# Kernel tuning notes

Hardware: AMD Instinct MI355X
Metric: run time of the kernel (lower is better)

## Reference

```python
import jax, jax.numpy as jnp
import numpy as np

NUM_CLS = 80
C = 256
IMG = 1024.0
N = 256
SR = 2  # sampling_ratio
MIN_SIZE = 16.0
SCALES = (0.25, 0.125, 0.0625, 0.03125)
HW = ((256, 256), (128, 128), (64, 64), (32, 32))


def _roialign(feat, rois, scale, out):
    # feat: [C, H, W]; rois: [n, 4] (y1, x1, y2, x2) in image coords.
    # torchvision-style ROIAlign (aligned=False), sampling_ratio=SR, avg pool.
    Cc, H, W = feat.shape
    n = rois.shape[0]
    y1 = rois[:, 0] * scale
    x1 = rois[:, 1] * scale
    rh = jnp.maximum(rois[:, 2] * scale - y1, 1.0)
    rw = jnp.maximum(rois[:, 3] * scale - x1, 1.0)
    # per-bin sample offsets: (bin + (s+0.5)/SR) * bin_size
    g = (jnp.arange(out, dtype=feat.dtype)[:, None]
         + (jnp.arange(SR, dtype=feat.dtype)[None, :] + 0.5) / SR).reshape(-1)  # [out*SR]
    ys = y1[:, None] + g[None, :] * (rh / out)[:, None]  # [n, out*SR]
    xs = x1[:, None] + g[None, :] * (rw / out)[:, None]
    S = out * SR
    yy = jnp.broadcast_to(ys[:, :, None], (n, S, S)).reshape(n, S * S)
    xx = jnp.broadcast_to(xs[:, None, :], (n, S, S)).reshape(n, S * S)
    valid = (yy > -1.0) & (yy < H) & (xx > -1.0) & (xx < W)
    yc = jnp.clip(yy, 0.0, H - 1.0)
    xc = jnp.clip(xx, 0.0, W - 1.0)
    y0 = jnp.floor(yc)
    x0 = jnp.floor(xc)
    ly = yc - y0
    lx = xc - x0
    y0i = y0.astype(jnp.int32)
    x0i = x0.astype(jnp.int32)
    y1i = jnp.minimum(y0i + 1, H - 1)
    x1i = jnp.minimum(x0i + 1, W - 1)
    f00 = feat[:, y0i, x0i]  # [C, n, S*S]
    f01 = feat[:, y0i, x1i]
    f10 = feat[:, y1i, x0i]
    f11 = feat[:, y1i, x1i]
    val = (f00 * (1 - ly) * (1 - lx) + f01 * (1 - ly) * lx
           + f10 * ly * (1 - lx) + f11 * ly * lx)
    val = jnp.where(valid[None], val, 0.0)
    val = val.reshape(Cc, n, out, SR, out, SR).mean(axis=(3, 5))
    return val.transpose(1, 0, 2, 3)  # [n, C, out, out]


def _pool(P, rois, out):
    # roi_layer: FPN level assignment via log2 of sqrt(area)/224, clamp to levels 0..3
    area = jnp.prod(rois[:, 2:4] - rois[:, 0:2] + 1.0, axis=-1)
    lvl = jnp.clip(jnp.floor(4.0 + jnp.log(jnp.sqrt(area) / 224.0) / np.log(2.0)), 2.0, 5.0) - 2.0
    lvl = lvl.astype(jnp.int32)
    pooled = jnp.zeros((rois.shape[0], C, out, out), dtype=rois.dtype)
    for l in range(4):
        pl = _roialign(P[l], rois, SCALES[l], out)
        pooled = pooled + jnp.where((lvl == l)[:, None, None, None], pl, 0.0)
    return pooled


def _loc2bbox(loc, anchor):
    chw = anchor[..., 2:4] - anchor[..., 0:2]
    cyx = anchor[..., 0:2] + chw * 0.5
    yx = loc[..., 0:2] * chw + cyx
    hw = jnp.exp(loc[..., 2:4]) * chw
    return jnp.concatenate([yx - hw * 0.5, yx + hw * 0.5], axis=-1)


def _head(x, W1, b1, W2, b2, Wc, bc, Wl, bl):
    x = x.reshape(x.shape[0], -1)
    h = jax.nn.relu(x @ W1 + b1)
    h = jax.nn.relu(h @ W2 + b2)
    return h @ Wc + bc, h @ Wl + bl


def _cascade(P, rois, params):
    stds = (jnp.array([0.1, 0.1, 0.2, 0.2], dtype=rois.dtype),
            jnp.array([0.05, 0.05, 0.1, 0.1], dtype=rois.dtype),
            jnp.array([1 / 30.0, 1 / 30.0, 1 / 15.0, 1 / 15.0], dtype=rois.dtype))
    roi = rois
    valid = jnp.ones((rois.shape[0],), dtype=bool)
    t = jnp.arange(rois.shape[0])
    pre_b = jnp.zeros((rois.shape[0], NUM_CLS, 4), dtype=rois.dtype)
    pre_s = jnp.zeros((rois.shape[0], NUM_CLS), dtype=rois.dtype)
    for s in range(3):
        x = _pool(P, roi, 7)
        logits, loc = _head(x, *params[s])
        loc = loc.reshape(-1, NUM_CLS + 1, 4)[:, 1:] * stds[s]
        boxes = _loc2bbox(loc, roi[:, None, :])  # [N, NUM_CLS, 4]
        score = jax.nn.softmax(logits, axis=-1)[:, 1:]
        pre_b = pre_b + boxes
        pre_s = pre_s + score
        best = jnp.argmax(score, axis=-1)
        roi = boxes[t, best]
        roi = jnp.clip(roi, 0.0, IMG)  # square image: clamp both coords to [0, IMG]
        if s < 2:  # original filters only after stages 1 and 2
            hw = roi[:, 2:4] - roi[:, 0:2]
            valid = valid & jnp.all(hw >= MIN_SIZE, axis=-1)
    m = valid.astype(pre_s.dtype)
    return pre_b / 3.0 * m[:, None, None], pre_s / 3.0 * m[:, None]


def setup_inputs():
    key = jax.random.key(0)
    ks = jax.random.split(key, 32)
    inp = {}
    for i, (h, w) in enumerate(HW):
        inp[f"P{i}"] = jax.random.normal(ks[i], (C, h, w), dtype=jnp.float32)
    yx1 = jax.random.uniform(ks[4], (N, 2), minval=0.0, maxval=IMG - 64.0)
    sz = jnp.exp(jax.random.uniform(ks[5], (N, 2), minval=np.log(16.0), maxval=np.log(600.0)))
    yx2 = jnp.clip(yx1 + sz, 0.0, IMG - 1.0)
    inp["rois"] = jnp.concatenate([yx1, yx2], axis=-1).astype(jnp.float32)
    dims = [(C * 49, 1024), (1024,), (1024, 1024), (1024,),
            (1024, NUM_CLS + 1), (NUM_CLS + 1,), (1024, (NUM_CLS + 1) * 4), ((NUM_CLS + 1) * 4,)]
    names = ["W1", "b1", "W2", "b2", "Wc", "bc", "Wl", "bl"]
    k = 6
    for s in range(3):
        for nm, d in zip(names, dims):
            if len(d) == 1:
                inp[f"s{s}_{nm}"] = jnp.zeros(d, dtype=jnp.float32)
            else:
                inp[f"s{s}_{nm}"] = 0.02 * jax.random.normal(ks[k], d, dtype=jnp.float32)
                k += 1
    return inp


def reference(P0, P1, P2, P3, rois,
              s0_W1, s0_b1, s0_W2, s0_b2, s0_Wc, s0_bc, s0_Wl, s0_bl,
              s1_W1, s1_b1, s1_W2, s1_b2, s1_Wc, s1_bc, s1_Wl, s1_bl,
              s2_W1, s2_b1, s2_W2, s2_b2, s2_Wc, s2_bc, s2_Wl, s2_bl):
    P = (P0, P1, P2, P3)
    params = [(s0_W1, s0_b1, s0_W2, s0_b2, s0_Wc, s0_bc, s0_Wl, s0_bl),
              (s1_W1, s1_b1, s1_W2, s1_b2, s1_Wc, s1_bc, s1_Wl, s1_bl),
              (s2_W1, s2_b1, s2_W2, s2_b2, s2_Wc, s2_bc, s2_Wl, s2_bl)]
    return _cascade(P, rois, params)
```

## Files before the change

kernel.cpp:

```cpp
#include <hip/hip_runtime.h>
#include <math.h>


#define NROI 256
#define NCLS 80
#define APITCH 40

typedef __attribute__((ext_vector_type(8))) short short8;
typedef __attribute__((ext_vector_type(4))) float f32x4;

__device__ __forceinline__ unsigned short f2bf(float f) {
  unsigned u = __builtin_bit_cast(unsigned, f);
  unsigned r = (u + 0x7FFFu + ((u >> 16) & 1u)) >> 16;
  return (unsigned short)r;
}
__device__ __forceinline__ float bf2f(unsigned short u) {
  return __builtin_bit_cast(float, (unsigned)u << 16);
}

__global__ __launch_bounds__(256) void prep_kernel(
    const float* __restrict__ P0, const float* __restrict__ P1,
    const float* __restrict__ P2, const float* __restrict__ P3,
    unsigned short* __restrict__ Pb0, unsigned short* __restrict__ Pb1,
    unsigned short* __restrict__ Pb2, unsigned short* __restrict__ Pb3,
    const float* __restrict__ W1a, const float* __restrict__ W1b,
    const float* __restrict__ W1c,
    const float* __restrict__ W2a, const float* __restrict__ W2b,
    const float* __restrict__ W2c,
    const float* __restrict__ Wca, const float* __restrict__ Wcb,
    const float* __restrict__ Wcc,
    const float* __restrict__ Wla, const float* __restrict__ Wlb,
    const float* __restrict__ Wlc,
    unsigned short* __restrict__ Wt1, unsigned short* __restrict__ Wt2,
    unsigned short* __restrict__ Wth) {
  __shared__ unsigned short lt[32][66];
  int bid = blockIdx.x;
  int t = threadIdx.x;
  int r0 = t >> 3;
  int c = t & 7;

  float4 v0, v1;
  unsigned short* D;
  size_t drow;
  int Kd;
  int k0;

  if (bid < 10880) {
    const float* S;
    int N, idx;
    if (bid < 8192)       { S = P0; D = Pb0; N = 65536; idx = bid; }
    else if (bid < 10240) { S = P1; D = Pb1; N = 16384; idx = bid - 8192; }
    else if (bid < 10752) { S = P2; D = Pb2; N = 4096;  idx = bid - 10240; }
    else                  { S = P3; D = Pb3; N = 1024;  idx = bid - 10752; }
    k0 = (idx & 3) * 64;
    int n0 = (idx >> 2) * 32;
    Kd = 256;
    drow = n0;
    const float* a = S + (size_t)(k0 + r0) * N + n0 + c * 4;
    v0 = *(const float4*)a;
    v1 = *(const float4*)(a + (size_t)32 * N);
  } else if (bid < 29696) {
    int idx = bid - 10880;
    int s = idx / 6272;
    idx -= s * 6272;
    const float* W = (s == 0) ? W1a : (s == 1) ? W1b : W1c;
    int kd0 = (idx % 196) * 64;
    int n0 = (idx / 196) * 32;
    int p = kd0 >> 8;
    int c0 = kd0 & 255;
    k0 = kd0;
    Kd = 12544;
    drow = n0;
    D = Wt1 + (size_t)s * 12544 * 1024;
    const float* a = W + (size_t)((c0 + r0) * 49 + p) * 1024 + n0 + c * 4;
    v0 = *(const float4*)a;
    v1 = *(const float4*)(a + (size_t)32 * 49 * 1024);
  } else if (bid < 31232) {
    int idx = bid - 29696;
    int s = idx >> 9;
    idx &= 511;
    const float* W = (s == 0) ? W2a : (s == 1) ? W2b : W2c;
    k0 = (idx & 15) * 64;
    int n0 = (idx >> 4) * 32;
    Kd = 1024;
    drow = n0;
    D = Wt2 + (size_t)s * 1024 * 1024;
    const float* a = W + (size_t)(k0 + r0) * 1024 + n0 + c * 4;
    v0 = *(const float4*)a;
    v1 = *(const float4*)(a + (size_t)32 * 1024);
  } else {
    int idx = bid - 31232;
    int s = idx >> 8;
    idx &= 255;
    const float* wc = (s == 0) ? Wca : (s == 1) ? Wcb : Wcc;
    const float* wl = (s == 0) ? Wla : (s == 1) ? Wlb : Wlc;
    k0 = (idx & 15) * 64;
    int n0 = (idx >> 4) * 32;
    Kd = 1024;
    drow = n0;
    D = Wth + (size_t)s * 512 * 1024;
    float a0[4], a1[4];
#pragma unroll
    for (int j = 0; j < 4; j++) {
      int nn = n0 + c * 4 + j;
      float x0 = 0.0f, x1 = 0.0f;
      if (nn < 81) {
        x0 = wc[(size_t)(k0 + r0) * 81 + nn];
        x1 = wc[(size_t)(k0 + r0 + 32) * 81 + nn];
      } else if (nn < 405) {
        x0 = wl[(size_t)(k0 + r0) * 324 + (nn - 81)];
        x1 = wl[(size_t)(k0 + r0 + 32) * 324 + (nn - 81)];
      }
      a0[j] = x0;
      a1[j] = x1;
    }
    v0.x = a0[0]; v0.y = a0[1]; v0.z = a0[2]; v0.w = a0[3];
    v1.x = a1[0]; v1.y = a1[1]; v1.z = a1[2]; v1.w = a1[3];
  }

  const float* pv0 = (const float*)&v0;
  const float* pv1 = (const float*)&v1;
#pragma unroll
  for (int j = 0; j < 4; j++) {
    lt[c * 4 + j][r0] = f2bf(pv0[j]);
    lt[c * 4 + j][r0 + 32] = f2bf(pv1[j]);
  }
  __syncthreads();

  int n = t >> 3;
  int k8 = (t & 7) * 8;
  const unsigned int* lrow = (const unsigned int*)&lt[n][k8];
  uint4 o;
  o.x = lrow[0];
  o.y = lrow[1];
  o.z = lrow[2];
  o.w = lrow[3];
  *(uint4*)(D + (drow + n) * (size_t)Kd + k0 + k8) = o;
}

__global__ __launch_bounds__(256) void pool_kernel2(
    const unsigned short* __restrict__ Pb0, const unsigned short* __restrict__ Pb1,
    const unsigned short* __restrict__ Pb2, const unsigned short* __restrict__ Pb3,
    const float* __restrict__ roi, unsigned short* __restrict__ pooled) {
  int t = threadIdx.x;
  int n = blockIdx.y;
  int p = blockIdx.x * 4 + (t >> 6);
  if (p >= 49) return;
  int lane = t & 63;
  int c4 = lane * 4;
  int py = p / 7, px = p % 7;

  float r0 = roi[n * 4 + 0];
  float r1 = roi[n * 4 + 1];
  float r2 = roi[n * 4 + 2];
  float r3 = roi[n * 4 + 3];

  float area = (r2 - r0 + 1.0f) * (r3 - r1 + 1.0f);
  float lf = floorf(4.0f + log2f(sqrtf(area) / 224.0f));
  lf = fminf(fmaxf(lf, 2.0f), 5.0f);
  int lvl = (int)lf - 2;

  float scale;
  int H;
  const unsigned short* fb;
  if (lvl == 0)      { scale = 0.25f;    H = 256; fb = Pb0; }
  else if (lvl == 1) { scale = 0.125f;   H = 128; fb = Pb1; }
  else if (lvl == 2) { scale = 0.0625f;  H = 64;  fb = Pb2; }
  else               { scale = 0.03125f; H = 32;  fb = Pb3; }
  int W = H;

  float y1 = r0 * scale;
  float x1 = r1 * scale;
  float rh = fmaxf(r2 * scale - y1, 1.0f);
  float rw = fmaxf(r3 * scale - x1, 1.0f);
  float bh = rh * (1.0f / 7.0f);
  float bw = rw * (1.0f / 7.0f);

  float a0 = 0.f, a1 = 0.f, a2 = 0.f, a3 = 0.f;
#pragma unroll
  for (int ry = 0; ry < 2; ry++) {
    float yy = y1 + ((float)py + ((float)ry + 0.5f) * 0.5f) * bh;
    bool vy = (yy > -1.0f) && (yy < (float)H);
    float ycl = fminf(fmaxf(yy, 0.0f), (float)(H - 1));
    float y0f = floorf(ycl);
    float ly = ycl - y0f;
    int y0i = (int)y0f;
    int y1i = min(y0i + 1, H - 1);
#pragma unroll
    for (int rx = 0; rx < 2; rx++) {
      float xx = x1 + ((float)px + ((float)rx + 0.5f) * 0.5f) * bw;
      bool vx = (xx > -1.0f) && (xx < (float)W);
      float xcl = fminf(fmaxf(xx, 0.0f), (float)(W - 1));
      float x0f = floorf(xcl);
      float lx = xcl - x0f;
      int x0i = (int)x0f;
      int x1i = min(x0i + 1, W - 1);
      float w00 = (1.f - ly) * (1.f - lx);
      float w01 = (1.f - ly) * lx;
      float w10 = ly * (1.f - lx);
      float w11 = ly * lx;
      if (!(vy && vx)) { w00 = w01 = w10 = w11 = 0.f; }
      ushort4 f00 = *(const ushort4*)(fb + ((size_t)(y0i * W + x0i) * 256 + c4));
      ushort4 f01 = *(const ushort4*)(fb + ((size_t)(y0i * W + x1i) * 256 + c4));
      ushort4 f10 = *(const ushort4*)(fb + ((size_t)(y1i * W + x0i) * 256 + c4));
      ushort4 f11 = *(const ushort4*)(fb + ((size_t)(y1i * W + x1i) * 256 + c4));
      a0 += bf2f(f00.x) * w00 + bf2f(f01.x) * w01 + bf2f(f10.x) * w10 + bf2f(f11.x) * w11;
      a1 += bf2f(f00.y) * w00 + bf2f(f01.y) * w01 + bf2f(f10.y) * w10 + bf2f(f11.y) * w11;
      a2 += bf2f(f00.z) * w00 + bf2f(f01.z) * w01 + bf2f(f10.z) * w10 + bf2f(f11.z) * w11;
      a3 += bf2f(f00.w) * w00 + bf2f(f01.w) * w01 + bf2f(f10.w) * w10 + bf2f(f11.w) * w11;
    }
  }
  ushort4 o;
  o.x = f2bf(a0 * 0.25f);
  o.y = f2bf(a1 * 0.25f);
  o.z = f2bf(a2 * 0.25f);
  o.w = f2bf(a3 * 0.25f);
  *(ushort4*)(pooled + (size_t)n * 12544 + p * 256 + c4) = o;
}

__global__ __launch_bounds__(256) void gemm_bf16(
    const unsigned short* __restrict__ A, const unsigned short* __restrict__ B,
    float* __restrict__ Cpart, int M, int N, int K, int iters) {
  __shared__ unsigned short As[128 * APITCH];
  __shared__ unsigned short Bs[128 * APITCH];
  const int t = threadIdx.x;
  const int n0 = blockIdx.x * 128;
  const int m0 = blockIdx.y * 128;
  const size_t kt0 = (size_t)blockIdx.z * iters * 32;

  const int row = t >> 2;
  const int off = (t & 3) * 8;
  const unsigned short* pa0 = A + (size_t)(m0 + row) * K + kt0 + off;
  const unsigned short* pa1 = pa0 + (size_t)64 * K;
  const unsigned short* pb0 = B + (size_t)(n0 + row) * K + kt0 + off;
  const unsigned short* pb1 = pb0 + (size_t)64 * K;

  const int lane = t & 63;
  const int wave = t >> 6;
  const int wm = (wave >> 1) * 64;
  const int wn = (wave & 1) * 64;
  const int fr = lane & 15;
  const int kq = (lane >> 4) * 8;

  f32x4 acc[4][4];
#pragma unroll
  for (int i = 0; i < 4; i++)
#pragma unroll
    for (int j = 0; j < 4; j++) acc[i][j] = (f32x4){0.f, 0.f, 0.f, 0.f};

  uint4 ra0 = *(const uint4*)pa0;
  uint4 ra1 = *(const uint4*)pa1;
  uint4 rb0 = *(const uint4*)pb0;
  uint4 rb1 = *(const uint4*)pb1;

  for (int it = 0; it < iters; ++it) {
    *(uint4*)&As[row * APITCH + off] = ra0;
    *(uint4*)&As[(row + 64) * APITCH + off] = ra1;
    *(uint4*)&Bs[row * APITCH + off] = rb0;
    *(uint4*)&Bs[(row + 64) * APITCH + off] = rb1;
    __syncthreads();
    if (it + 1 < iters) {
      int d = (it + 1) * 32;
      ra0 = *(const uint4*)(pa0 + d);
      ra1 = *(const uint4*)(pa1 + d);
      rb0 = *(const uint4*)(pb0 + d);
      rb1 = *(const uint4*)(pb1 + d);
    }
    short8 af[4], bfv[4];
#pragma unroll
    for (int f = 0; f < 4; f++)
      af[f] = *(const short8*)&As[(wm + f * 16 + fr) * APITCH + kq];
#pragma unroll
    for (int f = 0; f < 4; f++)
      bfv[f] = *(const short8*)&Bs[(wn + f * 16 + fr) * APITCH + kq];
#pragma unroll
    for (int fm = 0; fm < 4; fm++)
#pragma unroll
      for (int fn = 0; fn < 4; fn++)
        acc[fm][fn] = __builtin_amdgcn_mfma_f32_16x16x32_bf16(af[fm], bfv[fn],
                                                              acc[fm][fn], 0, 0, 0);
    __syncthreads();
  }

  float* Cp = Cpart + (size_t)blockIdx.z * M * N;
  const int colb = n0 + wn + fr;
  const int rowb = m0 + wm + (lane >> 4) * 4;
#pragma unroll
  for (int fm = 0; fm < 4; fm++)
#pragma unroll
    for (int fn = 0; fn < 4; fn++)
#pragma unroll
      for (int r = 0; r < 4; r++)
        Cp[(size_t)(rowb + fm * 16 + r) * N + (colb + fn * 16)] = acc[fm][fn][r];
}

__global__ __launch_bounds__(256) void reduce_bias_relu(
    const float* __restrict__ parts, int nparts, const float* __restrict__ bias,
    unsigned short* __restrict__ outb) {
  int i = blockIdx.x * 256 + threadIdx.x;
  float s = 0.0f;
  for (int p = 0; p < nparts; ++p) s += parts[(size_t)p * 262144 + i];
  s = fmaxf(s + bias[i & 1023], 0.0f);
  outb[i] = f2bf(s);
}

__global__ __launch_bounds__(128) void decode_kernel(
    const float* __restrict__ headp, const float* __restrict__ bc,
    const float* __restrict__ bl,
    const float* __restrict__ roi_in, float* __restrict__ roi_out,
    float* __restrict__ valid,
    float* __restrict__ pre_b, float* __restrict__ pre_s,
    float* __restrict__ out,
    float st0, float st1, float st2, float st3, int stage) {
  int n = blockIdx.x;
  int t = threadIdx.x;
  __shared__ float red[128];
  __shared__ int redi[128];
  __shared__ float sroi[4];
  __shared__ float boxes[NCLS][4];

  if (t < 4) sroi[t] = roi_in[n * 4 + t];
  float l = -INFINITY;
  if (t < 81) {
    float s = 0.f;
#pragma unroll
    for (int z = 0; z < 4; z++) s += headp[(size_t)z * 131072 + n * 512 + t];
    l = s + bc[t];
  }
  red[t] = l;
  __syncthreads();
#pragma unroll
  for (int s = 64; s > 0; s >>= 1) {
    if (t < s) red[t] = fmaxf(red[t], red[t + s]);
    __syncthreads();
  }
  float mx = red[0];
  __syncthreads();
  red[t] = (t < 81) ? expf(l - mx) : 0.0f;
  __syncthreads();
#pragma unroll
  for (int s = 64; s > 0; s >>= 1) {
    if (t < s) red[t] += red[t + s];
    __syncthreads();
  }
  float denom = red[0];
  __syncthreads();

  float score = -INFINITY;
  if (t < NCLS) {
    float lj = 0.f;
#pragma unroll
    for (int z = 0; z < 4; z++) lj += headp[(size_t)z * 131072 + n * 512 + (t + 1)];
    lj += bc[t + 1];
    score = expf(lj - mx) / denom;
    float lp[4];
#pragma unroll
    for (int j = 0; j < 4; j++) {
      float s = 0.f;
#pragma unroll
      for (int z = 0; z < 4; z++)
        s += headp[(size_t)z * 131072 + n * 512 + 81 + (t + 1) * 4 + j];
      lp[j] = s + bl[(t + 1) * 4 + j];
    }
    float dy = lp[0] * st0;
    float dx = lp[1] * st1;
    float dh = lp[2] * st2;
    float dw = lp[3] * st3;
    float h_ = sroi[2] - sroi[0];
    float w_ = sroi[3] - sroi[1];
    float cy = sroi[0] + h_ * 0.5f;
    float cx = sroi[1] + w_ * 0.5f;
    float ny = dy * h_ + cy;
    float nx = dx * w_ + cx;
    float nh = expf(dh) * h_;
    float nw = expf(dw) * w_;
    float b0 = ny - nh * 0.5f;
    float b1v = nx - nw * 0.5f;
    float b2v = ny + nh * 0.5f;
    float b3v = nx + nw * 0.5f;
    int o = (n * NCLS + t) * 4;
    if (stage == 0) {
      pre_b[o + 0] = b0;
      pre_b[o + 1] = b1v;
      pre_b[o + 2] = b2v;
      pre_b[o + 3] = b3v;
      pre_s[n * NCLS + t] = score;
    } else if (stage == 1) {
      pre_b[o + 0] += b0;
      pre_b[o + 1] += b1v;
      pre_b[o + 2] += b2v;
      pre_b[o + 3] += b3v;
      pre_s[n * NCLS + t] += score;
    } else {
      float vm = valid[n] * (1.0f / 3.0f);
      out[o + 0] = (pre_b[o + 0] + b0) * vm;
      out[o + 1] = (pre_b[o + 1] + b1v) * vm;
      out[o + 2] = (pre_b[o + 2] + b2v) * vm;
      out[o + 3] = (pre_b[o + 3] + b3v) * vm;
      out[NROI * NCLS * 4 + n * NCLS + t] = (pre_s[n * NCLS + t] + score) * vm;
    }
    if (stage < 2) {
      boxes[t][0] = b0;
      boxes[t][1] = b1v;
      boxes[t][2] = b2v;
      boxes[t][3] = b3v;
    }
  }
  if (stage < 2) {
    red[t] = score;
    redi[t] = t;
    __syncthreads();
    for (int s = 64; s > 0; s >>= 1) {
      if (t < s) {
        float o2 = red[t + s];
        int oi = redi[t + s];
        if (o2 > red[t] || (o2 == red[t] && oi < redi[t])) {
          red[t] = o2;
          redi[t] = oi;
        }
      }
      __syncthreads();
    }
    if (t == 0) {
      int best = redi[0];
      float ry1 = fminf(fmaxf(boxes[best][0], 0.0f), 1024.0f);
      float rx1 = fminf(fmaxf(boxes[best][1], 0.0f), 1024.0f);
      float ry2 = fminf(fmaxf(boxes[best][2], 0.0f), 1024.0f);
      float rx2 = fminf(fmaxf(boxes[best][3], 0.0f), 1024.0f);
      roi_out[n * 4 + 0] = ry1;
      roi_out[n * 4 + 1] = rx1;
      roi_out[n * 4 + 2] = ry2;
      roi_out[n * 4 + 3] = rx2;
      float hh = ry2 - ry1, ww = rx2 - rx1;
      bool ok = (hh >= 16.0f && ww >= 16.0f);
      if (stage == 0) valid[n] = ok ? 1.0f : 0.0f;
      else if (!ok) valid[n] = 0.0f;
    }
  }
}

extern "C" void kernel_launch(void* const* d_in, const int* in_sizes, int n_in,
                              void* d_out, int out_size, void* d_ws, size_t ws_size,
                              hipStream_t stream) {
  const float* P0 = (const float*)d_in[0];
  const float* P1 = (const float*)d_in[1];
  const float* P2 = (const float*)d_in[2];
  const float* P3 = (const float*)d_in[3];
  const float* rois = (const float*)d_in[4];
  float* out = (float*)d_out;
  float* ws = (float*)d_ws;

  float* roi   = ws;
  float* valid = roi + 1024;
  float* pre_b = valid + 256;
  float* pre_s = pre_b + 81920;
  float* part1 = pre_s + 20480;
  float* part2 = part1 + (size_t)14 * 262144;
  float* parth = part2 + (size_t)8 * 262144;
  unsigned short* pooledb = (unsigned short*)(parth + (size_t)4 * 131072);
  unsigned short* Wt1 = pooledb + (size_t)256 * 12544;
  unsigned short* Wt2 = Wt1 + (size_t)3 * 12544 * 1024;
  unsigned short* Wth = Wt2 + (size_t)3 * 1024 * 1024;
  unsigned short* h1b = Wth + (size_t)3 * 512 * 1024;
  unsigned short* h2b = h1b + (size_t)256 * 1024;
  unsigned short* Pb0 = h2b + (size_t)256 * 1024;
  unsigned short* Pb1 = Pb0 + (size_t)65536 * 256;
  unsigned short* Pb2 = Pb1 + (size_t)16384 * 256;
  unsigned short* Pb3 = Pb2 + (size_t)4096 * 256;

  prep_kernel<<<32000, 256, 0, stream>>>(
      P0, P1, P2, P3, Pb0, Pb1, Pb2, Pb3,
      (const float*)d_in[5 + 0 * 8 + 0], (const float*)d_in[5 + 1 * 8 + 0],
      (const float*)d_in[5 + 2 * 8 + 0],
      (const float*)d_in[5 + 0 * 8 + 2], (const float*)d_in[5 + 1 * 8 + 2],
      (const float*)d_in[5 + 2 * 8 + 2],
      (const float*)d_in[5 + 0 * 8 + 4], (const float*)d_in[5 + 1 * 8 + 4],
      (const float*)d_in[5 + 2 * 8 + 4],
      (const float*)d_in[5 + 0 * 8 + 6], (const float*)d_in[5 + 1 * 8 + 6],
      (const float*)d_in[5 + 2 * 8 + 6],
      Wt1, Wt2, Wth);

  const float stds[3][4] = {
      {0.1f, 0.1f, 0.2f, 0.2f},
      {0.05f, 0.05f, 0.1f, 0.1f},
      {1.0f / 30.0f, 1.0f / 30.0f, 1.0f / 15.0f, 1.0f / 15.0f}};

  for (int s = 0; s < 3; s++) {
    const float* b1 = (const float*)d_in[5 + s * 8 + 1];
    const float* b2 = (const float*)d_in[5 + s * 8 + 3];
    const float* bc = (const float*)d_in[5 + s * 8 + 5];
    const float* bl = (const float*)d_in[5 + s * 8 + 7];
    const float* roi_src = (s == 0) ? rois : roi;

    pool_kernel2<<<dim3(13, 256), 256, 0, stream>>>(Pb0, Pb1, Pb2, Pb3, roi_src,
                                                    pooledb);

    gemm_bf16<<<dim3(8, 2, 14), 256, 0, stream>>>(
        pooledb, Wt1 + (size_t)s * 12544 * 1024, part1, 256, 1024, 12544, 28);
    reduce_bias_relu<<<1024, 256, 0, stream>>>(part1, 14, b1, h1b);

    gemm_bf16<<<dim3(8, 2, 8), 256, 0, stream>>>(
        h1b, Wt2 + (size_t)s * 1024 * 1024, part2, 256, 1024, 1024, 4);
    reduce_bias_relu<<<1024, 256, 0, stream>>>(part2, 8, b2, h2b);

    gemm_bf16<<<dim3(4, 2, 4), 256, 0, stream>>>(
        h2b, Wth + (size_t)s * 512 * 1024, parth, 256, 512, 1024, 8);

    decode_kernel<<<256, 128, 0, stream>>>(parth, bc, bl, roi_src, roi, valid,
                                           pre_b, pre_s, out, stds[s][0],
                                           stds[s][1], stds[s][2], stds[s][3], s);
  }
}
```

Measured before the change: 478.1 us.

## Make prep kernel persistent with double-buffered LDS and prefetch of next tile

The transpose/convert prep kernel now runs as a persistent grid of 2048 blocks that loop over the 32000 tiles instead of one block per tile. Each iteration issues the global loads for the next tile before the barrier and the store of the current tile, using two shared-memory buffers so the next writes don't race with current reads. This aims to hide memory latency and cut block launch overhead, at the cost of more registers and fewer resident waves to hide latency.

```diff
diff --git a/kernel.cpp b/kernel.cpp
--- a/kernel.cpp
+++ b/kernel.cpp
@@ -5,6 +5,8 @@
 #define NROI 256
 #define NCLS 80
 #define APITCH 40
+#define NTILES 32000
+#define PREP_GRID 2048
 
 typedef __attribute__((ext_vector_type(8))) short short8;
 typedef __attribute__((ext_vector_type(4))) float f32x4;
@@ -17,6 +19,16 @@
 __device__ __forceinline__ float bf2f(unsigned short u) {
   return __builtin_bit_cast(float, (unsigned)u << 16);
 }
+
+struct PrepDesc {
+  const float* a0;
+  const float* a1;
+  unsigned short* dp;
+  const float* wc;
+  const float* wl;
+  int k0, n0;
+  int head;
+};
 
 __global__ __launch_bounds__(256) void prep_kernel(
     const float* __restrict__ P0, const float* __restrict__ P1,
@@ -33,109 +45,128 @@
     const float* __restrict__ Wlc,
     unsigned short* __restrict__ Wt1, unsigned short* __restrict__ Wt2,
     unsigned short* __restrict__ Wth) {
-  __shared__ unsigned short lt[32][66];
-  int bid = blockIdx.x;
-  int t = threadIdx.x;
-  int r0 = t >> 3;
-  int c = t & 7;
-
-  float4 v0, v1;
-  unsigned short* D;
-  size_t drow;
-  int Kd;
-  int k0;
-
-  if (bid < 10880) {
-    const float* S;
-    int N, idx;
-    if (bid < 8192)       { S = P0; D = Pb0; N = 65536; idx = bid; }
-    else if (bid < 10240) { S = P1; D = Pb1; N = 16384; idx = bid - 8192; }
-    else if (bid < 10752) { S = P2; D = Pb2; N = 4096;  idx = bid - 10240; }
-    else                  { S = P3; D = Pb3; N = 1024;  idx = bid - 10752; }
-    k0 = (idx & 3) * 64;
-    int n0 = (idx >> 2) * 32;
-    Kd = 256;
-    drow = n0;
-    const float* a = S + (size_t)(k0 + r0) * N + n0 + c * 4;
-    v0 = *(const float4*)a;
-    v1 = *(const float4*)(a + (size_t)32 * N);
-  } else if (bid < 29696) {
-    int idx = bid - 10880;
-    int s = idx / 6272;
-    idx -= s * 6272;
-    const float* W = (s == 0) ? W1a : (s == 1) ? W1b : W1c;
-    int kd0 = (idx % 196) * 64;
-    int n0 = (idx / 196) * 32;
-    int p = kd0 >> 8;
-    int c0 = kd0 & 255;
-    k0 = kd0;
-    Kd = 12544;
-    drow = n0;
-    D = Wt1 + (size_t)s * 12544 * 1024;
-    const float* a = W + (size_t)((c0 + r0) * 49 + p) * 1024 + n0 + c * 4;
-    v0 = *(const float4*)a;
-    v1 = *(const float4*)(a + (size_t)32 * 49 * 1024);
-  } else if (bid < 31232) {
-    int idx = bid - 29696;
-    int s = idx >> 9;
-    idx &= 511;
-    const float* W = (s == 0) ? W2a : (s == 1) ? W2b : W2c;
-    k0 = (idx & 15) * 64;
-    int n0 = (idx >> 4) * 32;
-    Kd = 1024;
-    drow = n0;
-    D = Wt2 + (size_t)s * 1024 * 1024;
-    const float* a = W + (size_t)(k0 + r0) * 1024 + n0 + c * 4;
-    v0 = *(const float4*)a;
-    v1 = *(const float4*)(a + (size_t)32 * 1024);
-  } else {
-    int idx = bid - 31232;
-    int s = idx >> 8;
-    idx &= 255;
-    const float* wc = (s == 0) ? Wca : (s == 1) ? Wcb : Wcc;
-    const float* wl = (s == 0) ? Wla : (s == 1) ? Wlb : Wlc;
-    k0 = (idx & 15) * 64;
-    int n0 = (idx >> 4) * 32;
-    Kd = 1024;
-    drow = n0;
-    D = Wth + (size_t)s * 512 * 1024;
-    float a0[4], a1[4];
+  __shared__ unsigned short lt[2][32][66];
+  const int t = threadIdx.x;
+  const int r0 = t >> 3;
+  const int c = t & 7;
+  const int sn = t >> 3;
+  const int sk8 = (t & 7) * 8;
+
+  auto desc = [&](int tile, PrepDesc& d) {
+    d.head = 0;
+    if (tile < 10880) {
+      const float* S;
+      unsigned short* D;
+      int N, idx;
+      if (tile < 8192)       { S = P0; D = Pb0; N = 65536; idx = tile; }
+      else if (tile < 10240) { S = P1; D = Pb1; N = 16384; idx = tile - 8192; }
+      else if (tile < 10752) { S = P2; D = Pb2; N = 4096;  idx = tile - 10240; }
+      else                   { S = P3; D = Pb3; N = 1024;  idx = tile - 10752; }
+      int k0 = (idx & 3) * 64;
+      int n0 = (idx >> 2) * 32;
+      d.a0 = S + (size_t)(k0 + r0) * N + n0 + c * 4;
+      d.a1 = d.a0 + (size_t)32 * N;
+      d.dp = D + (size_t)(n0 + sn) * 256 + k0 + sk8;
+    } else if (tile < 29696) {
+      int idx = tile - 10880;
+      int s = idx / 6272;
+      idx -= s * 6272;
+      const float* W = (s == 0) ? W1a : (s == 1) ? W1b : W1c;
+      int kd0 = (idx % 196) * 64;
+      int n0 = (idx / 196) * 32;
+      int p = kd0 >> 8;
+      int c0 = kd0 & 255;
+      d.a0 = W + (size_t)((c0 + r0) * 49 + p) * 1024 + n0 + c * 4;
+      d.a1 = d.a0 + (size_t)32 * 49 * 1024;
+      d.dp = Wt1 + (size_t)s * 12544 * 1024 + (size_t)(n0 + sn) * 12544 + kd0 + sk8;
+    } else if (tile < 31232) {
+      int idx = tile - 29696;
+      int s = idx >> 9;
+      idx &= 511;
+      const float* W = (s == 0) ? W2a : (s == 1) ? W2b : W2c;
+      int k0 = (idx & 15) * 64;
+      int n0 = (idx >> 4) * 32;
+      d.a0 = W + (size_t)(k0 + r0) * 1024 + n0 + c * 4;
+      d.a1 = d.a0 + (size_t)32 * 1024;
+      d.dp = Wt2 + (size_t)s * 1024 * 1024 + (size_t)(n0 + sn) * 1024 + k0 + sk8;
+    } else {
+      int idx = tile - 31232;
+      int s = idx >> 8;
+      idx &= 255;
+      d.head = 1;
+      d.wc = (s == 0) ? Wca : (s == 1) ? Wcb : Wcc;
+      d.wl = (s == 0) ? Wla : (s == 1) ? Wlb : Wlc;
+      d.k0 = (idx & 15) * 64;
+      d.n0 = (idx >> 4) * 32;
+      d.dp = Wth + (size_t)s * 512 * 1024 + (size_t)(d.n0 + sn) * 1024 + d.k0 + sk8;
+    }
+  };
+
+  auto loadv = [&](const PrepDesc& d, float4& v0, float4& v1) {
+    if (!d.head) {
+      v0 = *(const float4*)d.a0;
+      v1 = *(const float4*)d.a1;
+    } else {
+      float a0[4], a1[4];
+#pragma unroll
+      for (int j = 0; j < 4; j++) {
+        int nn = d.n0 + c * 4 + j;
+        float x0 = 0.0f, x1 = 0.0f;
+        if (nn < 81) {
+          x0 = d.wc[(size_t)(d.k0 + r0) * 81 + nn];
+          x1 = d.wc[(size_t)(d.k0 + r0 + 32) * 81 + nn];
+        } else if (nn < 405) {
+          x0 = d.wl[(size_t)(d.k0 + r0) * 324 + (nn - 81)];
+          x1 = d.wl[(size_t)(d.k0 + r0 + 32) * 324 + (nn - 81)];
+        }
+        a0[j] = x0;
+        a1[j] = x1;
+      }
+      v0 = make_float4(a0[0], a0[1], a0[2], a0[3]);
+      v1 = make_float4(a1[0], a1[1], a1[2], a1[3]);
+    }
+  };
+
+  int tile = blockIdx.x;
+  PrepDesc d = {};
+  float4 v0 = make_float4(0.f, 0.f, 0.f, 0.f);
+  float4 v1 = v0;
+  if (tile < NTILES) {
+    desc(tile, d);
+    loadv(d, v0, v1);
+  }
+  int buf = 0;
+  while (tile < NTILES) {
+    const float* p0 = (const float*)&v0;
+    const float* p1 = (const float*)&v1;
 #pragma unroll
     for (int j = 0; j < 4; j++) {
-      int nn = n0 + c * 4 + j;
-      float x0 = 0.0f, x1 = 0.0f;
-      if (nn < 81) {
-        x0 = wc[(size_t)(k0 + r0) * 81 + nn];
-        x1 = wc[(size_t)(k0 + r0 + 32) * 81 + nn];
-      } else if (nn < 405) {
-        x0 = wl[(size_t)(k0 + r0) * 324 + (nn - 81)];
-        x1 = wl[(size_t)(k0 + r0 + 32) * 324 + (nn - 81)];
-      }
-      a0[j] = x0;
-      a1[j] = x1;
-    }
-    v0.x = a0[0]; v0.y = a0[1]; v0.z = a0[2]; v0.w = a0[3];
-    v1.x = a1[0]; v1.y = a1[1]; v1.z = a1[2]; v1.w = a1[3];
-  }
-
-  const float* pv0 = (const float*)&v0;
-  const float* pv1 = (const float*)&v1;
-#pragma unroll
-  for (int j = 0; j < 4; j++) {
-    lt[c * 4 + j][r0] = f2bf(pv0[j]);
-    lt[c * 4 + j][r0 + 32] = f2bf(pv1[j]);
-  }
-  __syncthreads();
-
-  int n = t >> 3;
-  int k8 = (t & 7) * 8;
-  const unsigned int* lrow = (const unsigned int*)&lt[n][k8];
-  uint4 o;
-  o.x = lrow[0];
-  o.y = lrow[1];
-  o.z = lrow[2];
-  o.w = lrow[3];
-  *(uint4*)(D + (drow + n) * (size_t)Kd + k0 + k8) = o;
+      lt[buf][c * 4 + j][r0] = f2bf(p0[j]);
+      lt[buf][c * 4 + j][r0 + 32] = f2bf(p1[j]);
+    }
+    int next = tile + PREP_GRID;
+    PrepDesc dn = {};
+    float4 w0 = make_float4(0.f, 0.f, 0.f, 0.f);
+    float4 w1 = w0;
+    if (next < NTILES) {
+      desc(next, dn);
+      loadv(dn, w0, w1);
+    }
+    __syncthreads();
+    const unsigned int* lrow = (const unsigned int*)&lt[buf][sn][sk8];
+    uint4 o;
+    o.x = lrow[0];
+    o.y = lrow[1];
+    o.z = lrow[2];
+    o.w = lrow[3];
+    *(uint4*)d.dp = o;
+
+    d = dn;
+    v0 = w0;
+    v1 = w1;
+    buf ^= 1;
+    tile = next;
+  }
 }
 
 __global__ __launch_bounds__(256) void pool_kernel2(
@@ -468,7 +499,7 @@
   unsigned short* Pb2 = Pb1 + (size_t)16384 * 256;
   unsigned short* Pb3 = Pb2 + (size_t)4096 * 256;
 
-  prep_kernel<<<32000, 256, 0, stream>>>(
+  prep_kernel<<<PREP_GRID, 256, 0, stream>>>(
       P0, P1, P2, P3, Pb0, Pb1, Pb2, Pb3,
       (const float*)d_in[5 + 0 * 8 + 0], (const float*)d_in[5 + 1 * 8 + 0],
       (const float*)d_in[5 + 2 * 8 + 0],
```

Result: slower. 560.8 us (+17.3%).
